# Kernel optimization log

Hardware: AMD Instinct MI355X
Metric: run time of the kernel (lower is better)

The kernel has to match this reference:

```python
import jax, jax.numpy as jnp
import numpy as np

B, L, D_NODE, D_EDGE, H = 4, 256, 256, 128, 8
DK = D_NODE // H        # 32, per-head node dim
DE = D_EDGE // H        # 16, per-head edge dim
NEG_SLOPE = 0.2

# Static index maps replicating the torch loop indexing (including its j-1 off-by-one / wraparound bug)
_GIDX = np.arange(L - 1)[None, :] + (np.arange(L - 1)[None, :] >= np.arange(L)[:, None])  # [L, L-1]: j-values visited for row i (j != i, in order)
_PIDX = (np.arange(L) - 1) % (L - 1)   # [L]: torch uses attention_probs[:, j-1] for every j != i
_II = np.arange(L)[:, None]            # [L, 1]


def lrelu(x):
    return jnp.where(x >= 0, x, NEG_SLOPE * x)


def setup_inputs() -> dict:
    key = jax.random.key(0)
    ks = jax.random.split(key, 19)
    w = lambda k, s, sc=0.05: jax.random.normal(k, s, jnp.float32) * sc
    return dict(
        node=w(ks[0], (B, L, D_NODE), 1.0),
        edge=w(ks[1], (B, L, L, D_EDGE), 1.0),
        Wn_w=w(ks[2], (D_NODE, D_NODE)), Wn_b=w(ks[3], (D_NODE,)),
        Wh_w=w(ks[4], (DK, DK)), Wh_b=w(ks[5], (DK,)),
        We_w=w(ks[6], (D_EDGE, D_EDGE)), We_b=w(ks[7], (D_EDGE,)),
        Wn2_w=w(ks[8], (D_NODE, D_NODE)), Wn2_b=w(ks[9], (D_NODE,)),
        We2_w=w(ks[10], (D_EDGE, D_EDGE)), We2_b=w(ks[11], (D_EDGE,)),
        attn_w=w(ks[12], (2 * DK + DE,)),                  # attn_linear (no bias), input order [hi, hj, eij]
        edge_w=w(ks[13], (DE + 2 * DK, DE)), edge_b=w(ks[14], (DE,)),  # edge_linear, input order [eij, hi, hj]
        out_n_w=w(ks[15], (D_NODE, D_NODE)), out_n_b=w(ks[16], (D_NODE,)),
        out_e_w=w(ks[17], (D_EDGE, D_EDGE)), out_e_b=w(ks[18], (D_EDGE,)),
    )


def reference(node, edge, Wn_w, Wn_b, Wh_w, Wh_b, We_w, We_b, Wn2_w, Wn2_b,
              We2_w, We2_b, attn_w, edge_w, edge_b, out_n_w, out_n_b, out_e_w, out_e_b):
    node_p = (node @ Wn_w + Wn_b).reshape(B, L, H, DK)
    edge_p = (edge @ We_w + We_b).reshape(B, L, L, H, DE)

    # ---- node update (all heads at once) ----
    wq, wk, we = attn_w[:DK], attn_w[DK:2 * DK], attn_w[2 * DK:]
    si = jnp.einsum('bihd,d->bih', node_p, wq)
    sj = jnp.einsum('bjhd,d->bjh', node_p, wk)
    se = jnp.einsum('bijhd,d->bijh', edge_p, we)
    scores = si[:, :, None, :] + sj[:, None, :, :] + se          # [B,L,L,H], score(i,j)
    sc = scores[:, _II, _GIDX, :]                                 # [B,L,L-1,H]: j != i, loop order
    probs = jax.nn.softmax(lrelu(sc), axis=2)                     # softmax over the L-1 neighbors
    probs_pair = probs[:, :, _PIDX, :]                            # [B,L,L,H]: replicate probs[:, j-1]
    mask = (1.0 - jnp.eye(L, dtype=node.dtype))[None, :, :, None]
    Whh = jnp.einsum('bjhd,de->bjhe', node_p, Wh_w) + Wh_b        # Wh(hj), bias inside the sum
    agg = jnp.einsum('bijh,bjhe->bihe', probs_pair * mask, Whh)
    node_h = (node_p + lrelu(agg)).reshape(B, L, D_NODE)          # concat heads == reshape
    new_node = node_h @ out_n_w + out_n_b

    # ---- edge update ----
    node_p2 = (new_node @ Wn2_w + Wn2_b).reshape(B, L, H, DK)
    edge_p2 = (edge @ We2_w + We2_b).reshape(B, L, L, H, DE)
    w_e, w_i, w_j = edge_w[:DE], edge_w[DE:DE + DK], edge_w[DE + DK:]
    e_new = (jnp.einsum('bijhd,de->bijhe', edge_p2, w_e)
             + jnp.einsum('bihd,de->bihe', node_p2, w_i)[:, :, None]
             + jnp.einsum('bjhd,de->bjhe', node_p2, w_j)[:, None]
             + edge_b)
    e_new = e_new * mask[..., None]                               # diagonal stays zero (zeros_like init)
    new_edge = e_new.reshape(B, L, L, D_EDGE) @ out_e_w + out_e_b
    return new_node, new_edge
```

## Files before the change

### kernel.cpp

```cpp
#include <hip/hip_runtime.h>

#define Bb 4
#define Ll 256
#define NEG 0.2f

typedef __attribute__((ext_vector_type(8))) short short8;
typedef __attribute__((ext_vector_type(4))) float f32x4;
typedef __attribute__((ext_vector_type(4))) unsigned uint4v;

__device__ __forceinline__ float lrelu(float x) { return x >= 0.f ? x : NEG * x; }

__device__ __forceinline__ short f2bf(float x) {
  unsigned u = __builtin_bit_cast(unsigned, x);
  unsigned r = (u + 0x7FFFu + ((u >> 16) & 1u)) >> 16;
  return (short)r;
}

__device__ __forceinline__ unsigned pack2bf(float e, float o) {
  unsigned ue = __builtin_bit_cast(unsigned, e);
  unsigned uo = __builtin_bit_cast(unsigned, o);
  return ((ue + 0x8000u) >> 16) | ((uo + 0x8000u) & 0xFFFF0000u);
}

__global__ void prep_kernel(const float* We_w, const float* We_b, const float* attn_w,
                            const float* We2_w, const float* We2_b, const float* edge_w,
                            const float* edge_b, const float* out_e_w, const float* out_e_b,
                            short* Vbf, float* chg, float* c0g, short* Gt) {
  int blk = blockIdx.x;
  int t = threadIdx.x;
  if (blk < 128) {
    __shared__ float m2[128];
    int c = blk;
    int h = t >> 4, e = t & 15;
    float s = 0.f;
    for (int d = 0; d < 16; ++d) s += We2_w[c * 128 + h * 16 + d] * edge_w[d * 16 + e];
    m2[t] = s;
    __syncthreads();
    float g = 0.f;
    for (int f = 0; f < 128; ++f) g += m2[f] * out_e_w[f * 128 + t];
    Gt[t * 128 + c] = f2bf(g);
  } else {
    __shared__ float b2e[128];
    const float* we = attn_w + 64;
    for (int idx = t; idx < 1024; idx += 128) {
      int c = idx >> 3, h = idx & 7;
      float s = 0.f;
      for (int d = 0; d < 16; ++d) s += We_w[c * 128 + h * 16 + d] * we[d];
      Vbf[h * 128 + c] = f2bf(s);
      Vbf[(h + 8) * 128 + c] = 0;
    }
    if (t < 8) {
      float s = 0.f;
      for (int d = 0; d < 16; ++d) s += We_b[t * 16 + d] * we[d];
      chg[t] = s;
    }
    {
      int h = t >> 4, e = t & 15;
      float s = 0.f;
      for (int d = 0; d < 16; ++d) s += We2_b[h * 16 + d] * edge_w[d * 16 + e];
      b2e[t] = s + edge_b[e];
    }
    __syncthreads();
    float s = out_e_b[t];
    for (int f = 0; f < 128; ++f) s += b2e[f] * out_e_w[f * 128 + t];
    c0g[t] = s;
  }
}

__global__ __launch_bounds__(256) void pack_kernel(const float* __restrict__ edge,
                                                   short* __restrict__ ebf) {
  long base = (long)blockIdx.x * 256 + threadIdx.x;
#pragma unroll
  for (int it = 0; it < 8; ++it) {
    long g = base + (long)it * 524288;
    const float4* src = reinterpret_cast<const float4*>(edge + g * 8);
    float4 f0 = src[0];
    float4 f1 = src[1];
    uint4v u;
    u.x = pack2bf(f0.x, f0.y);
    u.y = pack2bf(f0.z, f0.w);
    u.z = pack2bf(f1.x, f1.y);
    u.w = pack2bf(f1.z, f1.w);
    *(uint4v*)(ebf + g * 8) = u;
  }
}

__global__ __launch_bounds__(256) void node_in_fused(
    const float* __restrict__ node, const float* __restrict__ Wn_w,
    const float* __restrict__ Wn_b, const float* __restrict__ Wh_w,
    const float* __restrict__ Wh_b, const float* __restrict__ attn_w,
    float* __restrict__ node_p, float* __restrict__ Whh, float* __restrict__ si,
    float* __restrict__ sj) {
  __shared__ float a[4][256];
  __shared__ float np[4][256];
  int t = threadIdx.x;
  int row0 = blockIdx.x * 4;
  for (int q = t; q < 1024; q += 256) a[q >> 8][q & 255] = node[(long)row0 * 256 + q];
  __syncthreads();
  float acc[4];
  float bvv = Wn_b[t];
#pragma unroll
  for (int r = 0; r < 4; ++r) acc[r] = bvv;
  for (int k = 0; k < 256; ++k) {
    float w = Wn_w[k * 256 + t];
#pragma unroll
    for (int r = 0; r < 4; ++r) acc[r] += a[r][k] * w;
  }
#pragma unroll
  for (int r = 0; r < 4; ++r) {
    node_p[(long)(row0 + r) * 256 + t] = acc[r];
    np[r][t] = acc[r];
  }
  __syncthreads();
  int h = t >> 5, e = t & 31;
  float wb2 = Wh_b[e];
#pragma unroll
  for (int r = 0; r < 4; ++r) {
    float s = wb2;
    for (int d = 0; d < 32; ++d) s += np[r][h * 32 + d] * Wh_w[d * 32 + e];
    Whh[(long)(row0 + r) * 256 + t] = s;
  }
  if (t < 64) {
    int r = t >> 4, idx = t & 15, hh = idx & 7;
    const float* w = attn_w + (idx < 8 ? 0 : 32);
    float s = 0.f;
    for (int d = 0; d < 32; ++d) s += np[r][hh * 32 + d] * w[d];
    ((idx < 8) ? si : sj)[(long)(row0 + r) * 8 + hh] = s;
  }
}

template <bool UE>
__global__ __launch_bounds__(256) void attn_fused(
    const float* __restrict__ node_p, const float* __restrict__ Whh,
    const float* __restrict__ si, const float* __restrict__ sj,
    const short* __restrict__ ebf, const float* __restrict__ edge,
    const short* __restrict__ Vbf, const float* __restrict__ chg,
    float* __restrict__ node_h) {
  __shared__ float sjl[2048];
  __shared__ float sel[2048];
  __shared__ float pl[2048];
  __shared__ float sil[8];
  int t = threadIdx.x, bi = blockIdx.x;
  int b = bi >> 8, i = bi & 255;
  for (int q = t; q < 2048; q += 256) sjl[q] = sj[(long)b * 2048 + q];
  if (t < 8) sil[t] = si[(long)bi * 8 + t];

  {
    int l = t & 63, w = t >> 6;
    int lc = l & 15, lq = l >> 4;
    short8 vb[4];
#pragma unroll
    for (int ks = 0; ks < 4; ++ks) vb[ks] = *(const short8*)(Vbf + lc * 128 + ks * 32 + lq * 8);
    f32x4 acc[4];
#pragma unroll
    for (int mf = 0; mf < 4; ++mf) acc[mf] = (f32x4){0.f, 0.f, 0.f, 0.f};
#pragma unroll
    for (int mf = 0; mf < 4; ++mf) {
      int row = w * 64 + mf * 16 + lc;
#pragma unroll
      for (int ks = 0; ks < 4; ++ks) {
        short8 av;
        if constexpr (UE) {
          av = *(const short8*)(ebf + (long)bi * 32768 + row * 128 + ks * 32 + lq * 8);
        } else {
          const float* ap = edge + (long)bi * 32768 + row * 128 + ks * 32 + lq * 8;
          float4 f0 = *(const float4*)ap;
          float4 f1 = *(const float4*)(ap + 4);
          uint4v u;
          u.x = pack2bf(f0.x, f0.y);
          u.y = pack2bf(f0.z, f0.w);
          u.z = pack2bf(f1.x, f1.y);
          u.w = pack2bf(f1.z, f1.w);
          av = __builtin_bit_cast(short8, u);
        }
        acc[mf] = __builtin_amdgcn_mfma_f32_16x16x32_bf16(vb[ks], av, acc[mf], 0, 0, 0);
      }
    }
    if (lq < 2) {
      f32x4 chv = *(const f32x4*)(chg + lq * 4);
#pragma unroll
      for (int mf = 0; mf < 4; ++mf) {
        int row = w * 64 + mf * 16 + lc;
        f32x4 v = acc[mf] + chv;
        *(f32x4*)(&sel[row * 8 + lq * 4]) = v;
      }
    }
  }
  __syncthreads();

  int g = t >> 5, l32 = t & 31;
  float sc[8];
  float mx = -1e30f;
#pragma unroll
  for (int m = 0; m < 8; ++m) {
    int k = l32 + 32 * m;
    float v = -1e30f;
    if (k < 255) {
      int jj = k + (k >= i ? 1 : 0);
      v = sil[g] + sjl[jj * 8 + g] + sel[jj * 8 + g];
      v = lrelu(v);
    }
    sc[m] = v;
    mx = fmaxf(mx, v);
  }
#pragma unroll
  for (int d = 16; d >= 1; d >>= 1) mx = fmaxf(mx, __shfl_xor(mx, d));
  float sum = 0.f;
#pragma unroll
  for (int m = 0; m < 8; ++m) {
    int k = l32 + 32 * m;
    float e = (k < 255) ? __expf(sc[m] - mx) : 0.f;
    sc[m] = e;
    sum += e;
  }
#pragma unroll
  for (int d = 16; d >= 1; d >>= 1) sum += __shfl_xor(sum, d);
  float inv = 1.f / sum;
#pragma unroll
  for (int m = 0; m < 8; ++m) {
    int k = l32 + 32 * m;
    if (k < 255) pl[k * 8 + g] = sc[m] * inv;
  }
  __syncthreads();

  int h = g;
  const float* wb = Whh + (long)b * 65536 + t;
  float acc0 = 0.f, acc1 = 0.f;
#pragma unroll 8
  for (int j = 0; j < 256; j += 2) {
    int k0 = (j == 0) ? 254 : (j - 1);
    int k1 = j;
    float w0 = (j == i) ? 0.f : pl[k0 * 8 + h];
    float w1 = (j + 1 == i) ? 0.f : pl[k1 * 8 + h];
    acc0 += w0 * wb[(long)j * 256];
    acc1 += w1 * wb[(long)(j + 1) * 256];
  }
  float acc = acc0 + acc1;
  float np = node_p[(long)bi * 256 + t];
  node_h[(long)bi * 256 + t] = np + lrelu(acc);
}

__global__ __launch_bounds__(256) void node_out_pq(
    const float* __restrict__ node_h, const float* __restrict__ out_n_w,
    const float* __restrict__ out_n_b, const float* __restrict__ Wn2_w,
    const float* __restrict__ Wn2_b, const float* __restrict__ edge_w,
    const float* __restrict__ out_e_w, float* __restrict__ out_node,
    float* __restrict__ Pg, float* __restrict__ Qg) {
  __shared__ float a[4][256];
  __shared__ float b2[4][256];
  __shared__ float ninj[4][256];
  int t = threadIdx.x;
  int row0 = blockIdx.x * 4;
  for (int q = t; q < 1024; q += 256) a[q >> 8][q & 255] = node_h[(long)row0 * 256 + q];
  __syncthreads();
  float acc[4];
  float bv1 = out_n_b[t];
#pragma unroll
  for (int r = 0; r < 4; ++r) acc[r] = bv1;
  for (int k = 0; k < 256; ++k) {
    float w = out_n_w[k * 256 + t];
#pragma unroll
    for (int r = 0; r < 4; ++r) acc[r] += a[r][k] * w;
  }
#pragma unroll
  for (int r = 0; r < 4; ++r) {
    out_node[(long)(row0 + r) * 256 + t] = acc[r];
    b2[r][t] = acc[r];
  }
  __syncthreads();
  float acc2[4];
  float bv2 = Wn2_b[t];
#pragma unroll
  for (int r = 0; r < 4; ++r) acc2[r] = bv2;
  for (int k = 0; k < 256; ++k) {
    float w = Wn2_w[k * 256 + t];
#pragma unroll
    for (int r = 0; r < 4; ++r) acc2[r] += b2[r][k] * w;
  }
#pragma unroll
  for (int r = 0; r < 4; ++r) a[r][t] = acc2[r];
  __syncthreads();
  {
    int f = t & 127, h = f >> 4, e = f & 15;
    const float* w = edge_w + 256 + (t >> 7) * 512;
#pragma unroll
    for (int r = 0; r < 4; ++r) {
      float s = 0.f;
      for (int d = 0; d < 32; ++d) s += a[r][h * 32 + d] * w[d * 16 + e];
      ninj[r][t] = s;
    }
  }
  __syncthreads();
  {
    int o = t & 127;
    int half = (t >> 7) * 128;
#pragma unroll
    for (int r = 0; r < 4; ++r) {
      float s = 0.f;
      const float* src = ninj[r] + half;
      for (int f = 0; f < 128; ++f) s += src[f] * out_e_w[f * 128 + o];
      ((t < 128) ? Pg : Qg)[(long)(row0 + r) * 128 + o] = s;
    }
  }
}

template <bool UE>
__global__ __launch_bounds__(256) void edge_out_kernel(
    const float* __restrict__ edge, const short* __restrict__ ebf,
    const short* __restrict__ Gt, const float* __restrict__ Pg,
    const float* __restrict__ Qg, const float* __restrict__ c0g,
    const float* __restrict__ oeb, float* __restrict__ out_edge) {
  int t = threadIdx.x;
  int l = t & 63, wid = t >> 6;
  int wm = wid >> 1, wn = wid & 1;
  int lc = l & 15, lq = l >> 4;

  long row0 = (long)blockIdx.x * 128;
  int b = (int)(row0 >> 16);
  int i = (int)((row0 >> 8) & 255);
  int j0 = (int)(row0 & 255);

  short8 bv[4][4];
#pragma unroll
  for (int ks = 0; ks < 4; ++ks)
#pragma unroll
    for (int nf = 0; nf < 4; ++nf)
      bv[ks][nf] = *(const short8*)(Gt + (wn * 64 + nf * 16 + lc) * 128 + ks * 32 + lq * 8);

  f32x4 acc[4][4];
#pragma unroll
  for (int mf = 0; mf < 4; ++mf)
#pragma unroll
    for (int nf = 0; nf < 4; ++nf) acc[mf][nf] = (f32x4){0.f, 0.f, 0.f, 0.f};

#pragma unroll
  for (int ks = 0; ks < 4; ++ks) {
    short8 av[4];
#pragma unroll
    for (int mf = 0; mf < 4; ++mf) {
      long row = row0 + wm * 64 + mf * 16 + lc;
      if constexpr (UE) {
        av[mf] = *(const short8*)(ebf + row * 128 + ks * 32 + lq * 8);
      } else {
        const float* ap = edge + row * 128 + ks * 32 + lq * 8;
        float4 f0 = *(const float4*)ap;
        float4 f1 = *(const float4*)(ap + 4);
        uint4v u;
        u.x = pack2bf(f0.x, f0.y);
        u.y = pack2bf(f0.z, f0.w);
        u.z = pack2bf(f1.x, f1.y);
        u.w = pack2bf(f1.z, f1.w);
        av[mf] = __builtin_bit_cast(short8, u);
      }
    }
#pragma unroll
    for (int mf = 0; mf < 4; ++mf)
#pragma unroll
      for (int nf = 0; nf < 4; ++nf)
        acc[mf][nf] =
            __builtin_amdgcn_mfma_f32_16x16x32_bf16(bv[ks][nf], av[mf], acc[mf][nf], 0, 0, 0);
  }

  f32x4 pc[4];
#pragma unroll
  for (int nf = 0; nf < 4; ++nf) {
    int cb = wn * 64 + nf * 16 + lq * 4;
    f32x4 p = *(const f32x4*)(Pg + ((long)(b * 256 + i)) * 128 + cb);
    f32x4 c0 = *(const f32x4*)(c0g + cb);
    pc[nf] = p + c0;
  }
#pragma unroll
  for (int mf = 0; mf < 4; ++mf) {
    int er = wm * 64 + mf * 16 + lc;
    int j = j0 + er;
    const float* Qrow = Qg + ((long)(b * 256 + j)) * 128;
    float* orow = out_edge + (row0 + er) * 128;
    if (j == i) {
#pragma unroll
      for (int nf = 0; nf < 4; ++nf) {
        int cb = wn * 64 + nf * 16 + lq * 4;
        f32x4 v = *(const f32x4*)(oeb + cb);
        __builtin_nontemporal_store(v, (f32x4*)(orow + cb));
      }
    } else {
#pragma unroll
      for (int nf = 0; nf < 4; ++nf) {
        int cb = wn * 64 + nf * 16 + lq * 4;
        f32x4 q4 = *(const f32x4*)(Qrow + cb);
        f32x4 v = acc[mf][nf] + pc[nf] + q4;
        __builtin_nontemporal_store(v, (f32x4*)(orow + cb));
      }
    }
  }
}

extern "C" void kernel_launch(void* const* d_in, const int* in_sizes, int n_in,
                              void* d_out, int out_size, void* d_ws, size_t ws_size,
                              hipStream_t stream) {
  const float* node = (const float*)d_in[0];
  const float* edge = (const float*)d_in[1];
  const float* Wn_w = (const float*)d_in[2];
  const float* Wn_b = (const float*)d_in[3];
  const float* Wh_w = (const float*)d_in[4];
  const float* Wh_b = (const float*)d_in[5];
  const float* We_w = (const float*)d_in[6];
  const float* We_b = (const float*)d_in[7];
  const float* Wn2_w = (const float*)d_in[8];
  const float* Wn2_b = (const float*)d_in[9];
  const float* We2_w = (const float*)d_in[10];
  const float* We2_b = (const float*)d_in[11];
  const float* attn_w = (const float*)d_in[12];
  const float* edge_w = (const float*)d_in[13];
  const float* edge_b = (const float*)d_in[14];
  const float* out_n_w = (const float*)d_in[15];
  const float* out_n_b = (const float*)d_in[16];
  const float* out_e_w = (const float*)d_in[17];
  const float* out_e_b = (const float*)d_in[18];

  float* out_node = (float*)d_out;
  float* out_edge = ((float*)d_out) + 262144;

  float* ws = (float*)d_ws;
  float* node_p = ws;
  float* Whh    = ws + 262144;
  float* node_h = ws + 524288;
  float* si     = ws + 786432;
  float* sjv    = ws + 794624;
  float* Pg     = ws + 802816;
  float* Qg     = ws + 933888;
  float* chg    = ws + 1064960;
  float* c0g    = ws + 1065088;
  short* Gt     = (short*)(ws + 1065216);
  short* Vbf    = (short*)(ws + 1073408);
  short* ebf    = (short*)(ws + 1074432);
  const bool big = ws_size >= (size_t)(1074432 + 16777216) * 4;

  prep_kernel<<<129, 128, 0, stream>>>(We_w, We_b, attn_w, We2_w, We2_b, edge_w, edge_b,
                                       out_e_w, out_e_b, Vbf, chg, c0g, Gt);
  node_in_fused<<<256, 256, 0, stream>>>(node, Wn_w, Wn_b, Wh_w, Wh_b, attn_w, node_p, Whh,
                                         si, sjv);
  if (big) {
    pack_kernel<<<2048, 256, 0, stream>>>(edge, ebf);
    attn_fused<true><<<1024, 256, 0, stream>>>(node_p, Whh, si, sjv, ebf, edge, Vbf, chg,
                                               node_h);
  } else {
    attn_fused<false><<<1024, 256, 0, stream>>>(node_p, Whh, si, sjv, ebf, edge, Vbf, chg,
                                                node_h);
  }
  node_out_pq<<<256, 256, 0, stream>>>(node_h, out_n_w, out_n_b, Wn2_w, Wn2_b, edge_w,
                                       out_e_w, out_node, Pg, Qg);
  if (big)
    edge_out_kernel<true><<<2048, 256, 0, stream>>>(edge, ebf, Gt, Pg, Qg, c0g, out_e_b,
                                                    out_edge);
  else
    edge_out_kernel<false><<<2048, 256, 0, stream>>>(edge, ebf, Gt, Pg, Qg, c0g, out_e_b,
                                                     out_edge);
}
```

Before: 171.0 us.

## Compute edge GEMM and attention edge scores in one pass, storing bf16 intermediate

Replaces the pack kernel with an edge_t_kernel that reads fp32 edge once and does two MFMA jobs: the edge-transform GEMM, kept as a bf16 intermediate, and the per-head edge attention scores. The attention kernel now just loads the precomputed scores, and the final edge kernel only adds the P/Q bias terms to the stored bf16 product. This removes the separate bf16 pack pass and the second edge read, in exchange for a 32MB bf16 intermediate write and read, an extra rounding of the GEMM result to bf16, and a larger workspace. Nontemporal stores on the output are also dropped.

```diff
diff --git a/kernel.cpp b/kernel.cpp
--- a/kernel.cpp
+++ b/kernel.cpp
@@ -20,6 +20,13 @@
   unsigned ue = __builtin_bit_cast(unsigned, e);
   unsigned uo = __builtin_bit_cast(unsigned, o);
   return ((ue + 0x8000u) >> 16) | ((uo + 0x8000u) & 0xFFFF0000u);
+}
+
+__device__ __forceinline__ float bflo(unsigned u) {
+  return __builtin_bit_cast(float, u << 16);
+}
+__device__ __forceinline__ float bfhi(unsigned u) {
+  return __builtin_bit_cast(float, u & 0xFFFF0000u);
 }
 
 __global__ void prep_kernel(const float* We_w, const float* We_b, const float* attn_w,
@@ -67,21 +74,89 @@
   }
 }
 
-__global__ __launch_bounds__(256) void pack_kernel(const float* __restrict__ edge,
-                                                   short* __restrict__ ebf) {
-  long base = (long)blockIdx.x * 256 + threadIdx.x;
-#pragma unroll
-  for (int it = 0; it < 8; ++it) {
-    long g = base + (long)it * 524288;
-    const float4* src = reinterpret_cast<const float4*>(edge + g * 8);
-    float4 f0 = src[0];
-    float4 f1 = src[1];
-    uint4v u;
-    u.x = pack2bf(f0.x, f0.y);
-    u.y = pack2bf(f0.z, f0.w);
-    u.z = pack2bf(f1.x, f1.y);
-    u.w = pack2bf(f1.z, f1.w);
-    *(uint4v*)(ebf + g * 8) = u;
+__global__ __launch_bounds__(256, 2) void edge_t_kernel(
+    const float* __restrict__ edge, const short* __restrict__ Gt,
+    const short* __restrict__ Vbf, const float* __restrict__ chg,
+    short* __restrict__ Tf, float* __restrict__ seg) {
+  int t = threadIdx.x;
+  int l = t & 63, wid = t >> 6;
+  int wm = wid >> 1, wn = wid & 1;
+  int lc = l & 15, lq = l >> 4;
+  long row0 = (long)blockIdx.x * 128;
+
+  short8 bv[4][4];
+#pragma unroll
+  for (int ks = 0; ks < 4; ++ks)
+#pragma unroll
+    for (int nf = 0; nf < 4; ++nf)
+      bv[ks][nf] = *(const short8*)(Gt + (wn * 64 + nf * 16 + lc) * 128 + ks * 32 + lq * 8);
+
+  short8 vb[4];
+#pragma unroll
+  for (int ks = 0; ks < 4; ++ks) vb[ks] = *(const short8*)(Vbf + lc * 128 + ks * 32 + lq * 8);
+
+  f32x4 accT[4][4];
+#pragma unroll
+  for (int mf = 0; mf < 4; ++mf)
+#pragma unroll
+    for (int nf = 0; nf < 4; ++nf) accT[mf][nf] = (f32x4){0.f, 0.f, 0.f, 0.f};
+  f32x4 accS[4];
+#pragma unroll
+  for (int mf = 0; mf < 4; ++mf) accS[mf] = (f32x4){0.f, 0.f, 0.f, 0.f};
+
+#pragma unroll
+  for (int ks = 0; ks < 4; ++ks) {
+    short8 av[4];
+#pragma unroll
+    for (int mf = 0; mf < 4; ++mf) {
+      const float* ap = edge + (row0 + wm * 64 + mf * 16 + lc) * 128 + ks * 32 + lq * 8;
+      float4 f0 = *(const float4*)ap;
+      float4 f1 = *(const float4*)(ap + 4);
+      uint4v u;
+      u.x = pack2bf(f0.x, f0.y);
+      u.y = pack2bf(f0.z, f0.w);
+      u.z = pack2bf(f1.x, f1.y);
+      u.w = pack2bf(f1.z, f1.w);
+      av[mf] = __builtin_bit_cast(short8, u);
+    }
+#pragma unroll
+    for (int mf = 0; mf < 4; ++mf)
+#pragma unroll
+      for (int nf = 0; nf < 4; ++nf)
+        accT[mf][nf] =
+            __builtin_amdgcn_mfma_f32_16x16x32_bf16(bv[ks][nf], av[mf], accT[mf][nf], 0, 0, 0);
+    if (wn == 0) {
+#pragma unroll
+      for (int mf = 0; mf < 4; ++mf)
+        accS[mf] = __builtin_amdgcn_mfma_f32_16x16x32_bf16(vb[ks], av[mf], accS[mf], 0, 0, 0);
+    }
+  }
+
+  short* tb = Tf + (long)blockIdx.x * 16384;
+#pragma unroll
+  for (int mf = 0; mf < 4; ++mf)
+#pragma unroll
+    for (int np = 0; np < 2; ++np) {
+      f32x4 a0 = accT[mf][2 * np];
+      f32x4 a1 = accT[mf][2 * np + 1];
+      uint4v u;
+      u.x = pack2bf(a0.x, a0.y);
+      u.y = pack2bf(a0.z, a0.w);
+      u.z = pack2bf(a1.x, a1.y);
+      u.w = pack2bf(a1.z, a1.w);
+      *(uint4v*)(tb + (mf * 2 + np) * 2048 + t * 8) = u;
+    }
+
+  if (wn == 0 && lq < 2) {
+    f32x4 chv = *(const f32x4*)(chg + lq * 4);
+    long slab = blockIdx.x >> 1;
+    int off = (blockIdx.x & 1) * 128;
+#pragma unroll
+    for (int mf = 0; mf < 4; ++mf) {
+      int lrow = off + wm * 64 + mf * 16 + lc;
+      f32x4 v = accS[mf] + chv;
+      *(f32x4*)(seg + slab * 2048 + lrow * 8 + lq * 4) = v;
+    }
   }
 }
 
@@ -129,13 +204,78 @@
   }
 }
 
-template <bool UE>
 __global__ __launch_bounds__(256) void attn_fused(
     const float* __restrict__ node_p, const float* __restrict__ Whh,
     const float* __restrict__ si, const float* __restrict__ sj,
-    const short* __restrict__ ebf, const float* __restrict__ edge,
-    const short* __restrict__ Vbf, const float* __restrict__ chg,
-    float* __restrict__ node_h) {
+    const float* __restrict__ seg, float* __restrict__ node_h) {
+  __shared__ float sjl[2048];
+  __shared__ float sel[2048];
+  __shared__ float pl[2048];
+  __shared__ float sil[8];
+  int t = threadIdx.x, bi = blockIdx.x;
+  int b = bi >> 8, i = bi & 255;
+  for (int q = t; q < 2048; q += 256) sjl[q] = sj[(long)b * 2048 + q];
+  for (int q = t; q < 2048; q += 256) sel[q] = seg[(long)bi * 2048 + q];
+  if (t < 8) sil[t] = si[(long)bi * 8 + t];
+  __syncthreads();
+
+  int g = t >> 5, l32 = t & 31;
+  float sc[8];
+  float mx = -1e30f;
+#pragma unroll
+  for (int m = 0; m < 8; ++m) {
+    int k = l32 + 32 * m;
+    float v = -1e30f;
+    if (k < 255) {
+      int jj = k + (k >= i ? 1 : 0);
+      v = sil[g] + sjl[jj * 8 + g] + sel[jj * 8 + g];
+      v = lrelu(v);
+    }
+    sc[m] = v;
+    mx = fmaxf(mx, v);
+  }
+#pragma unroll
+  for (int d = 16; d >= 1; d >>= 1) mx = fmaxf(mx, __shfl_xor(mx, d));
+  float sum = 0.f;
+#pragma unroll
+  for (int m = 0; m < 8; ++m) {
+    int k = l32 + 32 * m;
+    float e = (k < 255) ? __expf(sc[m] - mx) : 0.f;
+    sc[m] = e;
+    sum += e;
+  }
+#pragma unroll
+  for (int d = 16; d >= 1; d >>= 1) sum += __shfl_xor(sum, d);
+  float inv = 1.f / sum;
+#pragma unroll
+  for (int m = 0; m < 8; ++m) {
+    int k = l32 + 32 * m;
+    if (k < 255) pl[k * 8 + g] = sc[m] * inv;
+  }
+  __syncthreads();
+
+  int h = g;
+  const float* wb = Whh + (long)b * 65536 + t;
+  float acc0 = 0.f, acc1 = 0.f;
+#pragma unroll 8
+  for (int j = 0; j < 256; j += 2) {
+    int k0 = (j == 0) ? 254 : (j - 1);
+    int k1 = j;
+    float w0 = (j == i) ? 0.f : pl[k0 * 8 + h];
+    float w1 = (j + 1 == i) ? 0.f : pl[k1 * 8 + h];
+    acc0 += w0 * wb[(long)j * 256];
+    acc1 += w1 * wb[(long)(j + 1) * 256];
+  }
+  float acc = acc0 + acc1;
+  float np = node_p[(long)bi * 256 + t];
+  node_h[(long)bi * 256 + t] = np + lrelu(acc);
+}
+
+__global__ __launch_bounds__(256) void attn_fallback(
+    const float* __restrict__ node_p, const float* __restrict__ Whh,
+    const float* __restrict__ si, const float* __restrict__ sj,
+    const float* __restrict__ edge, const short* __restrict__ Vbf,
+    const float* __restrict__ chg, float* __restrict__ node_h) {
   __shared__ float sjl[2048];
   __shared__ float sel[2048];
   __shared__ float pl[2048];
@@ -144,7 +284,6 @@
   int b = bi >> 8, i = bi & 255;
   for (int q = t; q < 2048; q += 256) sjl[q] = sj[(long)b * 2048 + q];
   if (t < 8) sil[t] = si[(long)bi * 8 + t];
-
   {
     int l = t & 63, w = t >> 6;
     int lc = l & 15, lq = l >> 4;
@@ -159,21 +298,16 @@
       int row = w * 64 + mf * 16 + lc;
 #pragma unroll
       for (int ks = 0; ks < 4; ++ks) {
-        short8 av;
-        if constexpr (UE) {
-          av = *(const short8*)(ebf + (long)bi * 32768 + row * 128 + ks * 32 + lq * 8);
-        } else {
-          const float* ap = edge + (long)bi * 32768 + row * 128 + ks * 32 + lq * 8;
-          float4 f0 = *(const float4*)ap;
-          float4 f1 = *(const float4*)(ap + 4);
-          uint4v u;
-          u.x = pack2bf(f0.x, f0.y);
-          u.y = pack2bf(f0.z, f0.w);
-          u.z = pack2bf(f1.x, f1.y);
-          u.w = pack2bf(f1.z, f1.w);
-          av = __builtin_bit_cast(short8, u);
-        }
-        acc[mf] = __builtin_amdgcn_mfma_f32_16x16x32_bf16(vb[ks], av, acc[mf], 0, 0, 0);
+        const float* ap = edge + (long)bi * 32768 + row * 128 + ks * 32 + lq * 8;
+        float4 f0 = *(const float4*)ap;
+        float4 f1 = *(const float4*)(ap + 4);
+        uint4v u;
+        u.x = pack2bf(f0.x, f0.y);
+        u.y = pack2bf(f0.z, f0.w);
+        u.z = pack2bf(f1.x, f1.y);
+        u.w = pack2bf(f1.z, f1.w);
+        acc[mf] = __builtin_amdgcn_mfma_f32_16x16x32_bf16(vb[ks], __builtin_bit_cast(short8, u),
+                                                          acc[mf], 0, 0, 0);
       }
     }
     if (lq < 2) {
@@ -187,7 +321,6 @@
     }
   }
   __syncthreads();
-
   int g = t >> 5, l32 = t & 31;
   float sc[8];
   float mx = -1e30f;
@@ -222,7 +355,6 @@
     if (k < 255) pl[k * 8 + g] = sc[m] * inv;
   }
   __syncthreads();
-
   int h = g;
   const float* wb = Whh + (long)b * 65536 + t;
   float acc0 = 0.f, acc1 = 0.f;
@@ -304,62 +436,23 @@
   }
 }
 
-template <bool UE>
-__global__ __launch_bounds__(256) void edge_out_kernel(
-    const float* __restrict__ edge, const short* __restrict__ ebf,
-    const short* __restrict__ Gt, const float* __restrict__ Pg,
+__global__ __launch_bounds__(256) void edge_final_kernel(
+    const short* __restrict__ Tf, const float* __restrict__ Pg,
     const float* __restrict__ Qg, const float* __restrict__ c0g,
     const float* __restrict__ oeb, float* __restrict__ out_edge) {
   int t = threadIdx.x;
   int l = t & 63, wid = t >> 6;
   int wm = wid >> 1, wn = wid & 1;
   int lc = l & 15, lq = l >> 4;
-
   long row0 = (long)blockIdx.x * 128;
   int b = (int)(row0 >> 16);
   int i = (int)((row0 >> 8) & 255);
   int j0 = (int)(row0 & 255);
 
-  short8 bv[4][4];
-#pragma unroll
-  for (int ks = 0; ks < 4; ++ks)
-#pragma unroll
-    for (int nf = 0; nf < 4; ++nf)
-      bv[ks][nf] = *(const short8*)(Gt + (wn * 64 + nf * 16 + lc) * 128 + ks * 32 + lq * 8);
-
-  f32x4 acc[4][4];
-#pragma unroll
-  for (int mf = 0; mf < 4; ++mf)
-#pragma unroll
-    for (int nf = 0; nf < 4; ++nf) acc[mf][nf] = (f32x4){0.f, 0.f, 0.f, 0.f};
-
-#pragma unroll
-  for (int ks = 0; ks < 4; ++ks) {
-    short8 av[4];
-#pragma unroll
-    for (int mf = 0; mf < 4; ++mf) {
-      long row = row0 + wm * 64 + mf * 16 + lc;
-      if constexpr (UE) {
-        av[mf] = *(const short8*)(ebf + row * 128 + ks * 32 + lq * 8);
-      } else {
-        const float* ap = edge + row * 128 + ks * 32 + lq * 8;
-        float4 f0 = *(const float4*)ap;
-        float4 f1 = *(const float4*)(ap + 4);
-        uint4v u;
-        u.x = pack2bf(f0.x, f0.y);
-        u.y = pack2bf(f0.z, f0.w);
-        u.z = pack2bf(f1.x, f1.y);
-        u.w = pack2bf(f1.z, f1.w);
-        av[mf] = __builtin_bit_cast(short8, u);
-      }
-    }
-#pragma unroll
-    for (int mf = 0; mf < 4; ++mf)
-#pragma unroll
-      for (int nf = 0; nf < 4; ++nf)
-        acc[mf][nf] =
-            __builtin_amdgcn_mfma_f32_16x16x32_bf16(bv[ks][nf], av[mf], acc[mf][nf], 0, 0, 0);
-  }
+  const short* tb = Tf + (long)blockIdx.x * 16384;
+  uint4v u[8];
+#pragma unroll
+  for (int q = 0; q < 8; ++q) u[q] = *(const uint4v*)(tb + q * 2048 + t * 8);
 
   f32x4 pc[4];
 #pragma unroll
@@ -369,6 +462,7 @@
     f32x4 c0 = *(const f32x4*)(c0g + cb);
     pc[nf] = p + c0;
   }
+
 #pragma unroll
   for (int mf = 0; mf < 4; ++mf) {
     int er = wm * 64 + mf * 16 + lc;
@@ -379,16 +473,102 @@
 #pragma unroll
       for (int nf = 0; nf < 4; ++nf) {
         int cb = wn * 64 + nf * 16 + lq * 4;
-        f32x4 v = *(const f32x4*)(oeb + cb);
-        __builtin_nontemporal_store(v, (f32x4*)(orow + cb));
+        *(f32x4*)(orow + cb) = *(const f32x4*)(oeb + cb);
+      }
+    } else {
+#pragma unroll
+      for (int np = 0; np < 2; ++np) {
+        uint4v uu = u[mf * 2 + np];
+        f32x4 v0 = {bflo(uu.x), bfhi(uu.x), bflo(uu.y), bfhi(uu.y)};
+        f32x4 v1 = {bflo(uu.z), bfhi(uu.z), bflo(uu.w), bfhi(uu.w)};
+        int nf0 = 2 * np, nf1 = 2 * np + 1;
+        int cb0 = wn * 64 + nf0 * 16 + lq * 4;
+        int cb1 = wn * 64 + nf1 * 16 + lq * 4;
+        f32x4 q0 = *(const f32x4*)(Qrow + cb0);
+        f32x4 q1 = *(const f32x4*)(Qrow + cb1);
+        *(f32x4*)(orow + cb0) = v0 + pc[nf0] + q0;
+        *(f32x4*)(orow + cb1) = v1 + pc[nf1] + q1;
+      }
+    }
+  }
+}
+
+__global__ __launch_bounds__(256, 2) void edge_out_fallback(
+    const float* __restrict__ edge, const short* __restrict__ Gt,
+    const float* __restrict__ Pg, const float* __restrict__ Qg,
+    const float* __restrict__ c0g, const float* __restrict__ oeb,
+    float* __restrict__ out_edge) {
+  int t = threadIdx.x;
+  int l = t & 63, wid = t >> 6;
+  int wm = wid >> 1, wn = wid & 1;
+  int lc = l & 15, lq = l >> 4;
+  long row0 = (long)blockIdx.x * 128;
+  int b = (int)(row0 >> 16);
+  int i = (int)((row0 >> 8) & 255);
+  int j0 = (int)(row0 & 255);
+
+  short8 bv[4][4];
+#pragma unroll
+  for (int ks = 0; ks < 4; ++ks)
+#pragma unroll
+    for (int nf = 0; nf < 4; ++nf)
+      bv[ks][nf] = *(const short8*)(Gt + (wn * 64 + nf * 16 + lc) * 128 + ks * 32 + lq * 8);
+
+  f32x4 acc[4][4];
+#pragma unroll
+  for (int mf = 0; mf < 4; ++mf)
+#pragma unroll
+    for (int nf = 0; nf < 4; ++nf) acc[mf][nf] = (f32x4){0.f, 0.f, 0.f, 0.f};
+
+#pragma unroll
+  for (int ks = 0; ks < 4; ++ks) {
+    short8 av[4];
+#pragma unroll
+    for (int mf = 0; mf < 4; ++mf) {
+      const float* ap = edge + (row0 + wm * 64 + mf * 16 + lc) * 128 + ks * 32 + lq * 8;
+      float4 f0 = *(const float4*)ap;
+      float4 f1 = *(const float4*)(ap + 4);
+      uint4v u;
+      u.x = pack2bf(f0.x, f0.y);
+      u.y = pack2bf(f0.z, f0.w);
+      u.z = pack2bf(f1.x, f1.y);
+      u.w = pack2bf(f1.z, f1.w);
+      av[mf] = __builtin_bit_cast(short8, u);
+    }
+#pragma unroll
+    for (int mf = 0; mf < 4; ++mf)
+#pragma unroll
+      for (int nf = 0; nf < 4; ++nf)
+        acc[mf][nf] =
+            __builtin_amdgcn_mfma_f32_16x16x32_bf16(bv[ks][nf], av[mf], acc[mf][nf], 0, 0, 0);
+  }
+
+  f32x4 pc[4];
+#pragma unroll
+  for (int nf = 0; nf < 4; ++nf) {
+    int cb = wn * 64 + nf * 16 + lq * 4;
+    f32x4 p = *(const f32x4*)(Pg + ((long)(b * 256 + i)) * 128 + cb);
+    f32x4 c0 = *(const f32x4*)(c0g + cb);
+    pc[nf] = p + c0;
+  }
+#pragma unroll
+  for (int mf = 0; mf < 4; ++mf) {
+    int er = wm * 64 + mf * 16 + lc;
+    int j = j0 + er;
+    const float* Qrow = Qg + ((long)(b * 256 + j)) * 128;
+    float* orow = out_edge + (row0 + er) * 128;
+    if (j == i) {
+#pragma unroll
+      for (int nf = 0; nf < 4; ++nf) {
+        int cb = wn * 64 + nf * 16 + lq * 4;
+        *(f32x4*)(orow + cb) = *(const f32x4*)(oeb + cb);
       }
     } else {
 #pragma unroll
       for (int nf = 0; nf < 4; ++nf) {
         int cb = wn * 64 + nf * 16 + lq * 4;
         f32x4 q4 = *(const f32x4*)(Qrow + cb);
-        f32x4 v = acc[mf][nf] + pc[nf] + q4;
-        __builtin_nontemporal_store(v, (f32x4*)(orow + cb));
+        *(f32x4*)(orow + cb) = acc[mf][nf] + pc[nf] + q4;
       }
     }
   }
@@ -432,27 +612,24 @@
   float* c0g    = ws + 1065088;
   short* Gt     = (short*)(ws + 1065216);
   short* Vbf    = (short*)(ws + 1073408);
-  short* ebf    = (short*)(ws + 1074432);
-  const bool big = ws_size >= (size_t)(1074432 + 16777216) * 4;
+  float* seg    = ws + 1074432;
+  short* Tf     = (short*)(ws + 3171584);
+  const bool big = ws_size >= (size_t)(3171584 + 16777216) * 4;
 
   prep_kernel<<<129, 128, 0, stream>>>(We_w, We_b, attn_w, We2_w, We2_b, edge_w, edge_b,
                                        out_e_w, out_e_b, Vbf, chg, c0g, Gt);
   node_in_fused<<<256, 256, 0, stream>>>(node, Wn_w, Wn_b, Wh_w, Wh_b, attn_w, node_p, Whh,
                                          si, sjv);
   if (big) {
-    pack_kernel<<<2048, 256, 0, stream>>>(edge, ebf);
-    attn_fused<true><<<1024, 256, 0, stream>>>(node_p, Whh, si, sjv, ebf, edge, Vbf, chg,
-                                               node_h);
+    edge_t_kernel<<<2048, 256, 0, stream>>>(edge, Gt, Vbf, chg, Tf, seg);
+    attn_fused<<<1024, 256, 0, stream>>>(node_p, Whh, si, sjv, seg, node_h);
+    node_out_pq<<<256, 256, 0, stream>>>(node_h, out_n_w, out_n_b, Wn2_w, Wn2_b, edge_w,
+                                         out_e_w, out_node, Pg, Qg);
+    edge_final_kernel<<<2048, 256, 0, stream>>>(Tf, Pg, Qg, c0g, out_e_b, out_edge);
   } else {
-    attn_fused<false><<<1024, 256, 0, stream>>>(node_p, Whh, si, sjv, ebf, edge, Vbf, chg,
-                                                node_h);
-  }
-  node_out_pq<<<256, 256, 0, stream>>>(node_h, out_n_w, out_n_b, Wn2_w, Wn2_b, edge_w,
-                                       out_e_w, out_node, Pg, Qg);
-  if (big)
-    edge_out_kernel<true><<<2048, 256, 0, stream>>>(edge, ebf, Gt, Pg, Qg, c0g, out_e_b,
-                                                    out_edge);
-  else
-    edge_out_kernel<false><<<2048, 256, 0, stream>>>(edge, ebf, Gt, Pg, Qg, c0g, out_e_b,
-                                                     out_edge);
-}
+    attn_fallback<<<1024, 256, 0, stream>>>(node_p, Whh, si, sjv, edge, Vbf, chg, node_h);
+    node_out_pq<<<256, 256, 0, stream>>>(node_h, out_n_w, out_n_b, Wn2_w, Wn2_b, edge_w,
+                                         out_e_w, out_node, Pg, Qg);
+    edge_out_fallback<<<2048, 256, 0, stream>>>(edge, Gt, Pg, Qg, c0g, out_e_b, out_edge);
+  }
+}
```

Measured after the change: 177.3 us. +3.7%, slower.
